# Kernel tuning notes

Measured on AMD Instinct MI355X. Metric: run time of the kernel, lower is better.

Reference implementation:

```python
import jax, jax.numpy as jnp
import numpy as np

SCALE = 0.125  # quantization scale applied inline in the custom matmul
PAD = 4
STRIDE = 1


def setup_inputs() -> dict:
    key = jax.random.key(0)
    k1, k2, k3 = jax.random.split(key, 3)
    x = jax.random.normal(k1, (8, 64, 16384), dtype=jnp.float32)        # (N, C, L)
    weight = jax.random.normal(k2, (64, 64, 9), dtype=jnp.float32) * 0.05  # (O, I, K)
    bias = jax.random.normal(k3, (64,), dtype=jnp.float32)               # (O,)
    return {"x": x, "weight": weight, "bias": bias}


def reference(x, weight, bias):
    # Mathematically identical to: im2col unfold -> (N, out_l, C*K) @ (C*K, O),
    # then out * scale + bias. Expressed as a fused conv to avoid the huge
    # intermediate while computing the same result.
    out = jax.lax.conv_general_dilated(
        x, weight,
        window_strides=(STRIDE,),
        padding=[(PAD, PAD)],
        dimension_numbers=("NCH", "OIH", "NCH"),
    )  # (N, O, out_l)
    return out * SCALE + bias[None, :, None]
```

## Files before the change

kernel.cpp:

```cpp
#include <hip/hip_runtime.h>
#include <hip/hip_bf16.h>

#define C_IN    64
#define L_IN    16384
#define O_OUT   64
#define KTAP    9
#define LTILE   256
#define ROWS    272
#define RSTRIDE 72

typedef short          bf16x8 __attribute__((ext_vector_type(8)));
typedef unsigned short u16x8  __attribute__((ext_vector_type(8)));
typedef unsigned int   u32x4  __attribute__((ext_vector_type(4)));
typedef float          f32x4  __attribute__((ext_vector_type(4)));
typedef float          f32x8v __attribute__((ext_vector_type(8)));

static __device__ __forceinline__ unsigned short f2bf(float f) {
  __hip_bfloat16 h = __float2bfloat16(f);
  return __builtin_bit_cast(unsigned short, h);
}

static __device__ __forceinline__ unsigned int pk2(float lo, float hi) {
  return (unsigned int)f2bf(lo) | ((unsigned int)f2bf(hi) << 16);
}

__global__ void w_rearrange(const float* __restrict__ w,
                            unsigned short* __restrict__ w2) {
    int i = blockIdx.x * 256 + threadIdx.x;
    if (i >= KTAP * O_OUT * C_IN) return;
    int t  = i >> 12;
    int oc = i & 4095;
    w2[i] = f2bf(w[oc * KTAP + t] * 0.125f);
}

__global__ __launch_bounds__(256) void qconv_kernel(
    const float* __restrict__ x,
    const unsigned short* __restrict__ w2,
    const float* __restrict__ bias,
    float* __restrict__ out) {

  __shared__ __align__(16) unsigned short xs[ROWS][RSTRIDE];

  const int tid = threadIdx.x;
  const int n   = blockIdx.x >> 6;
  const int l0  = (blockIdx.x & 63) << 8;
  const float* xn = x + (size_t)n * C_IN * L_IN;

  for (int idx = tid; idx < ROWS; idx += 256) {
    const int cb = idx & 7;
    const int lb = idx >> 3;
    const int c0 = cb << 3;
    const int gl0 = l0 - 8 + (lb << 3);
    if (gl0 >= 0 && gl0 + 8 <= L_IN) {
      f32x8v v[8];
#pragma unroll
      for (int i = 0; i < 8; ++i)
        v[i] = *reinterpret_cast<const f32x8v*>(xn + (size_t)(c0 + i) * L_IN + gl0);
#pragma unroll
      for (int j = 0; j < 8; ++j) {
        u32x4 wv;
#pragma unroll
        for (int p = 0; p < 4; ++p)
          wv[p] = pk2(v[2 * p][j], v[2 * p + 1][j]);
        *reinterpret_cast<u32x4*>(&xs[(lb << 3) + j][c0]) = wv;
      }
    } else {
      unsigned short vb[8][8];
      for (int i = 0; i < 8; ++i)
        for (int j = 0; j < 8; ++j) {
          int gl = gl0 + j;
          vb[i][j] = (gl >= 0 && gl < L_IN)
                         ? f2bf(xn[(size_t)(c0 + i) * L_IN + gl])
                         : (unsigned short)0;
        }
      for (int j = 0; j < 8; ++j) {
        u16x8 wv;
        for (int i = 0; i < 8; ++i) wv[i] = vb[i][j];
        *reinterpret_cast<u16x8*>(&xs[(lb << 3) + j][c0]) = wv;
      }
    }
  }
  __syncthreads();

  const int wave = tid >> 6;
  const int lane = tid & 63;
  const int wr   = wave >> 1;
  const int wc   = wave & 1;
  const int col  = lane & 15;
  const int quad = lane >> 4;

  f32x4 acc[2][8];
#pragma unroll
  for (int m = 0; m < 2; ++m)
#pragma unroll
    for (int lt = 0; lt < 8; ++lt) acc[m][lt] = (f32x4){0.f, 0.f, 0.f, 0.f};

  const int rbase = (wc << 7) + col + 4;

  for (int t = 0; t < KTAP; ++t) {
    bf16x8 a[2][2];
#pragma unroll
    for (int m = 0; m < 2; ++m)
#pragma unroll
      for (int k = 0; k < 2; ++k)
        a[m][k] = *reinterpret_cast<const bf16x8*>(
            w2 + (t << 12) + (((wr << 5) + (m << 4) + col) << 6) + (k << 5) + (quad << 3));

#pragma unroll
    for (int k = 0; k < 2; ++k) {
#pragma unroll
      for (int lt = 0; lt < 8; ++lt) {
        const int r = rbase + t + (lt << 4);
        const bf16x8 b = *reinterpret_cast<const bf16x8*>(&xs[r][(k << 5) + (quad << 3)]);
        acc[0][lt] = __builtin_amdgcn_mfma_f32_16x16x32_bf16(a[0][k], b, acc[0][lt], 0, 0, 0);
        acc[1][lt] = __builtin_amdgcn_mfma_f32_16x16x32_bf16(a[1][k], b, acc[1][lt], 0, 0, 0);
      }
    }
  }

#pragma unroll
  for (int m = 0; m < 2; ++m) {
    const int obase = (wr << 5) + (m << 4) + (quad << 2);
    float bv[4];
#pragma unroll
    for (int reg = 0; reg < 4; ++reg) bv[reg] = bias[obase + reg];
#pragma unroll
    for (int lt = 0; lt < 8; ++lt) {
      const int l = l0 + (wc << 7) + (lt << 4) + col;
#pragma unroll
      for (int reg = 0; reg < 4; ++reg) {
        const int o = obase + reg;
        out[((size_t)(n * O_OUT + o) << 14) + l] = acc[m][lt][reg] + bv[reg];
      }
    }
  }
}

extern "C" void kernel_launch(void* const* d_in, const int* in_sizes, int n_in,
                              void* d_out, int out_size, void* d_ws, size_t ws_size,
                              hipStream_t stream) {
  const float*    x    = (const float*)d_in[0];
  const float*    w    = (const float*)d_in[1];
  const float*    bias = (const float*)d_in[2];
  float*          out  = (float*)d_out;
  unsigned short* w2   = (unsigned short*)d_ws;

  w_rearrange<<<(KTAP * O_OUT * C_IN + 255) / 256, 256, 0, stream>>>(w, w2);

  qconv_kernel<<<8 * (L_IN / LTILE), 256, 0, stream>>>(x, w2, bias, out);
}
```

Before: 98.83 us.

## Split L tile into two halves and overlap second-half staging with first-half MFMAs

```diff
diff --git a/kernel.cpp b/kernel.cpp
--- a/kernel.cpp
+++ b/kernel.cpp
@@ -7,13 +7,12 @@
 #define KTAP    9
 #define LTILE   256
 #define ROWS    272
+#define AROWS   144
 #define RSTRIDE 72
 
 typedef short          bf16x8 __attribute__((ext_vector_type(8)));
-typedef unsigned short u16x8  __attribute__((ext_vector_type(8)));
 typedef unsigned int   u32x4  __attribute__((ext_vector_type(4)));
 typedef float          f32x4  __attribute__((ext_vector_type(4)));
-typedef float          f32x8v __attribute__((ext_vector_type(8)));
 
 static __device__ __forceinline__ unsigned short f2bf(float f) {
   __hip_bfloat16 h = __float2bfloat16(f);
@@ -46,93 +45,165 @@
   const int l0  = (blockIdx.x & 63) << 8;
   const float* xn = x + (size_t)n * C_IN * L_IN;
 
-  for (int idx = tid; idx < ROWS; idx += 256) {
-    const int cb = idx & 7;
-    const int lb = idx >> 3;
-    const int c0 = cb << 3;
-    const int gl0 = l0 - 8 + (lb << 3);
-    if (gl0 >= 0 && gl0 + 8 <= L_IN) {
-      f32x8v v[8];
-#pragma unroll
-      for (int i = 0; i < 8; ++i)
-        v[i] = *reinterpret_cast<const f32x8v*>(xn + (size_t)(c0 + i) * L_IN + gl0);
-#pragma unroll
-      for (int j = 0; j < 8; ++j) {
-        u32x4 wv;
-#pragma unroll
-        for (int p = 0; p < 4; ++p)
-          wv[p] = pk2(v[2 * p][j], v[2 * p + 1][j]);
-        *reinterpret_cast<u32x4*>(&xs[(lb << 3) + j][c0]) = wv;
-      }
-    } else {
-      unsigned short vb[8][8];
-      for (int i = 0; i < 8; ++i)
-        for (int j = 0; j < 8; ++j) {
-          int gl = gl0 + j;
-          vb[i][j] = (gl >= 0 && gl < L_IN)
-                         ? f2bf(xn[(size_t)(c0 + i) * L_IN + gl])
-                         : (unsigned short)0;
+  const int ucb = tid & 7;
+  const int ulb = tid >> 3;
+  const int uc0 = ucb << 3;
+
+  const int a0_gl0 = l0 - 8 + (ulb << 2);
+  const bool a0_ok = (a0_gl0 >= 0) && (a0_gl0 + 4 <= L_IN);
+  f32x4 va0[8];
+  if (a0_ok) {
+#pragma unroll
+    for (int i = 0; i < 8; ++i)
+      va0[i] = *reinterpret_cast<const f32x4*>(xn + (size_t)(uc0 + i) * L_IN + a0_gl0);
+  }
+  const bool have1 = (tid < 32);
+  const int a1_gl0 = l0 - 8 + ((32 + ulb) << 2);
+  f32x4 va1[8];
+  if (have1) {
+#pragma unroll
+    for (int i = 0; i < 8; ++i)
+      va1[i] = *reinterpret_cast<const f32x4*>(xn + (size_t)(uc0 + i) * L_IN + a1_gl0);
+  }
+  const int b_gl0 = l0 + 136 + (ulb << 2);
+  const bool b_ok = (b_gl0 + 4 <= L_IN);
+  f32x4 vb[8];
+  if (b_ok) {
+#pragma unroll
+    for (int i = 0; i < 8; ++i)
+      vb[i] = *reinterpret_cast<const f32x4*>(xn + (size_t)(uc0 + i) * L_IN + b_gl0);
+  }
+
+  if (a0_ok) {
+#pragma unroll
+    for (int j = 0; j < 4; ++j) {
+      u32x4 wv;
+#pragma unroll
+      for (int p = 0; p < 4; ++p)
+        wv[p] = pk2(va0[2 * p][j], va0[2 * p + 1][j]);
+      *reinterpret_cast<u32x4*>(&xs[(ulb << 2) + j][uc0]) = wv;
+    }
+  } else {
+#pragma unroll
+    for (int j = 0; j < 4; ++j) {
+      const int gl = a0_gl0 + j;
+      u32x4 wv;
+#pragma unroll
+      for (int p = 0; p < 4; ++p) {
+        float lo = 0.f, hi = 0.f;
+        if (gl >= 0 && gl < L_IN) {
+          lo = xn[(size_t)(uc0 + 2 * p)     * L_IN + gl];
+          hi = xn[(size_t)(uc0 + 2 * p + 1) * L_IN + gl];
         }
-      for (int j = 0; j < 8; ++j) {
-        u16x8 wv;
-        for (int i = 0; i < 8; ++i) wv[i] = vb[i][j];
-        *reinterpret_cast<u16x8*>(&xs[(lb << 3) + j][c0]) = wv;
-      }
+        wv[p] = pk2(lo, hi);
+      }
+      *reinterpret_cast<u32x4*>(&xs[(ulb << 2) + j][uc0]) = wv;
+    }
+  }
+  if (have1) {
+#pragma unroll
+    for (int j = 0; j < 4; ++j) {
+      u32x4 wv;
+#pragma unroll
+      for (int p = 0; p < 4; ++p)
+        wv[p] = pk2(va1[2 * p][j], va1[2 * p + 1][j]);
+      *reinterpret_cast<u32x4*>(&xs[128 + (ulb << 2) + j][uc0]) = wv;
     }
   }
   __syncthreads();
 
   const int wave = tid >> 6;
   const int lane = tid & 63;
-  const int wr   = wave >> 1;
-  const int wc   = wave & 1;
   const int col  = lane & 15;
   const int quad = lane >> 4;
 
-  f32x4 acc[2][8];
-#pragma unroll
-  for (int m = 0; m < 2; ++m)
-#pragma unroll
-    for (int lt = 0; lt < 8; ++lt) acc[m][lt] = (f32x4){0.f, 0.f, 0.f, 0.f};
-
-  const int rbase = (wc << 7) + col + 4;
+  const unsigned short* wbase = w2 + (((wave << 4) + col) << 6) + (quad << 3);
+  const int obase = (wave << 4) + (quad << 2);
+  float bv[4];
+#pragma unroll
+  for (int reg = 0; reg < 4; ++reg) bv[reg] = bias[obase + reg];
+
+  f32x4 acc[8];
+#pragma unroll
+  for (int lt = 0; lt < 8; ++lt) acc[lt] = (f32x4){0.f, 0.f, 0.f, 0.f};
 
   for (int t = 0; t < KTAP; ++t) {
-    bf16x8 a[2][2];
-#pragma unroll
-    for (int m = 0; m < 2; ++m)
-#pragma unroll
-      for (int k = 0; k < 2; ++k)
-        a[m][k] = *reinterpret_cast<const bf16x8*>(
-            w2 + (t << 12) + (((wr << 5) + (m << 4) + col) << 6) + (k << 5) + (quad << 3));
-
+    bf16x8 a[2];
+#pragma unroll
+    for (int k = 0; k < 2; ++k)
+      a[k] = *reinterpret_cast<const bf16x8*>(wbase + (t << 12) + (k << 5));
 #pragma unroll
     for (int k = 0; k < 2; ++k) {
 #pragma unroll
       for (int lt = 0; lt < 8; ++lt) {
-        const int r = rbase + t + (lt << 4);
+        const int r = col + t + 4 + (lt << 4);
         const bf16x8 b = *reinterpret_cast<const bf16x8*>(&xs[r][(k << 5) + (quad << 3)]);
-        acc[0][lt] = __builtin_amdgcn_mfma_f32_16x16x32_bf16(a[0][k], b, acc[0][lt], 0, 0, 0);
-        acc[1][lt] = __builtin_amdgcn_mfma_f32_16x16x32_bf16(a[1][k], b, acc[1][lt], 0, 0, 0);
-      }
-    }
-  }
-
-#pragma unroll
-  for (int m = 0; m < 2; ++m) {
-    const int obase = (wr << 5) + (m << 4) + (quad << 2);
-    float bv[4];
-#pragma unroll
-    for (int reg = 0; reg < 4; ++reg) bv[reg] = bias[obase + reg];
-#pragma unroll
-    for (int lt = 0; lt < 8; ++lt) {
-      const int l = l0 + (wc << 7) + (lt << 4) + col;
-#pragma unroll
-      for (int reg = 0; reg < 4; ++reg) {
-        const int o = obase + reg;
-        out[((size_t)(n * O_OUT + o) << 14) + l] = acc[m][lt][reg] + bv[reg];
-      }
-    }
+        acc[lt] = __builtin_amdgcn_mfma_f32_16x16x32_bf16(a[k], b, acc[lt], 0, 0, 0);
+      }
+    }
+  }
+
+  if (b_ok) {
+#pragma unroll
+    for (int j = 0; j < 4; ++j) {
+      u32x4 wv;
+#pragma unroll
+      for (int p = 0; p < 4; ++p)
+        wv[p] = pk2(vb[2 * p][j], vb[2 * p + 1][j]);
+      *reinterpret_cast<u32x4*>(&xs[144 + (ulb << 2) + j][uc0]) = wv;
+    }
+  } else {
+#pragma unroll
+    for (int j = 0; j < 4; ++j) {
+      const int gl = b_gl0 + j;
+      u32x4 wv;
+#pragma unroll
+      for (int p = 0; p < 4; ++p) {
+        float lo = 0.f, hi = 0.f;
+        if (gl < L_IN) {
+          lo = xn[(size_t)(uc0 + 2 * p)     * L_IN + gl];
+          hi = xn[(size_t)(uc0 + 2 * p + 1) * L_IN + gl];
+        }
+        wv[p] = pk2(lo, hi);
+      }
+      *reinterpret_cast<u32x4*>(&xs[144 + (ulb << 2) + j][uc0]) = wv;
+    }
+  }
+  __syncthreads();
+
+#pragma unroll
+  for (int lt = 0; lt < 8; ++lt) {
+    const int l = l0 + (lt << 4) + col;
+#pragma unroll
+    for (int reg = 0; reg < 4; ++reg)
+      out[((size_t)(n * O_OUT + obase + reg) << 14) + l] = acc[lt][reg] + bv[reg];
+  }
+
+#pragma unroll
+  for (int lt = 0; lt < 8; ++lt) acc[lt] = (f32x4){0.f, 0.f, 0.f, 0.f};
+
+  for (int t = 0; t < KTAP; ++t) {
+    bf16x8 a[2];
+#pragma unroll
+    for (int k = 0; k < 2; ++k)
+      a[k] = *reinterpret_cast<const bf16x8*>(wbase + (t << 12) + (k << 5));
+#pragma unroll
+    for (int k = 0; k < 2; ++k) {
+#pragma unroll
+      for (int lt = 0; lt < 8; ++lt) {
+        const int r = 128 + col + t + 4 + (lt << 4);
+        const bf16x8 b = *reinterpret_cast<const bf16x8*>(&xs[r][(k << 5) + (quad << 3)]);
+        acc[lt] = __builtin_amdgcn_mfma_f32_16x16x32_bf16(a[k], b, acc[lt], 0, 0, 0);
+      }
+    }
+  }
+
+#pragma unroll
+  for (int lt = 0; lt < 8; ++lt) {
+    const int l = l0 + 128 + (lt << 4) + col;
+#pragma unroll
+    for (int reg = 0; reg < 4; ++reg)
+      out[((size_t)(n * O_OUT + obase + reg) << 14) + l] = acc[lt][reg] + bv[reg];
   }
 }
 
```

New measurement: 98.00 us. About the same (-0.8%).

## Fuse weight conversion into conv kernel and keep weight fragments in registers

Applied to the files above, without the earlier changes.

```diff
diff --git a/kernel.cpp b/kernel.cpp
--- a/kernel.cpp
+++ b/kernel.cpp
@@ -24,18 +24,9 @@
   return (unsigned int)f2bf(lo) | ((unsigned int)f2bf(hi) << 16);
 }
 
-__global__ void w_rearrange(const float* __restrict__ w,
-                            unsigned short* __restrict__ w2) {
-    int i = blockIdx.x * 256 + threadIdx.x;
-    if (i >= KTAP * O_OUT * C_IN) return;
-    int t  = i >> 12;
-    int oc = i & 4095;
-    w2[i] = f2bf(w[oc * KTAP + t] * 0.125f);
-}
-
 __global__ __launch_bounds__(256) void qconv_kernel(
     const float* __restrict__ x,
-    const unsigned short* __restrict__ w2,
+    const float* __restrict__ w,
     const float* __restrict__ bias,
     float* __restrict__ out) {
 
@@ -81,71 +72,105 @@
     }
   }
   __syncthreads();
+  __builtin_amdgcn_sched_barrier(0);
 
   const int wave = tid >> 6;
   const int lane = tid & 63;
-  const int wr   = wave >> 1;
-  const int wc   = wave & 1;
   const int col  = lane & 15;
   const int quad = lane >> 4;
+  const int o16  = (wave << 4) + col;
 
-  f32x4 acc[2][8];
+  u32x4 afr[2 * KTAP];
+  {
+    const float* wrow = w + (size_t)o16 * (C_IN * KTAP);
 #pragma unroll
-  for (int m = 0; m < 2; ++m)
+    for (int k = 0; k < 2; ++k) {
+      const float* wp = wrow + ((k << 5) + (quad << 3)) * KTAP;
+      f32x4 wt[18];
 #pragma unroll
-    for (int lt = 0; lt < 8; ++lt) acc[m][lt] = (f32x4){0.f, 0.f, 0.f, 0.f};
+      for (int j = 0; j < 18; ++j)
+        wt[j] = *reinterpret_cast<const f32x4*>(wp + 4 * j);
+#pragma unroll
+      for (int t = 0; t < KTAP; ++t) {
+        u32x4 fr;
+#pragma unroll
+        for (int p = 0; p < 4; ++p) {
+          const int e0 = (2 * p) * KTAP + t;
+          const int e1 = (2 * p + 1) * KTAP + t;
+          fr[p] = pk2(wt[e0 >> 2][e0 & 3] * 0.125f,
+                      wt[e1 >> 2][e1 & 3] * 0.125f);
+        }
+        afr[(t << 1) + k] = fr;
+      }
+    }
+  }
+  __builtin_amdgcn_sched_barrier(0);
 
-  const int rbase = (wc << 7) + col + 4;
+  const int obase = (wave << 4) + (quad << 2);
+  float bv[4];
+#pragma unroll
+  for (int reg = 0; reg < 4; ++reg) bv[reg] = bias[obase + reg];
 
-  for (int t = 0; t < KTAP; ++t) {
-    bf16x8 a[2][2];
+  f32x4 acc[8];
 #pragma unroll
-    for (int m = 0; m < 2; ++m)
-#pragma unroll
-      for (int k = 0; k < 2; ++k)
-        a[m][k] = *reinterpret_cast<const bf16x8*>(
-            w2 + (t << 12) + (((wr << 5) + (m << 4) + col) << 6) + (k << 5) + (quad << 3));
+  for (int lt = 0; lt < 8; ++lt) acc[lt] = (f32x4){0.f, 0.f, 0.f, 0.f};
 
 #pragma unroll
+  for (int t = 0; t < KTAP; ++t) {
+#pragma unroll
     for (int k = 0; k < 2; ++k) {
+      const bf16x8 a = __builtin_bit_cast(bf16x8, afr[(t << 1) + k]);
 #pragma unroll
       for (int lt = 0; lt < 8; ++lt) {
-        const int r = rbase + t + (lt << 4);
+        const int r = col + t + 4 + (lt << 4);
         const bf16x8 b = *reinterpret_cast<const bf16x8*>(&xs[r][(k << 5) + (quad << 3)]);
-        acc[0][lt] = __builtin_amdgcn_mfma_f32_16x16x32_bf16(a[0][k], b, acc[0][lt], 0, 0, 0);
-        acc[1][lt] = __builtin_amdgcn_mfma_f32_16x16x32_bf16(a[1][k], b, acc[1][lt], 0, 0, 0);
+        acc[lt] = __builtin_amdgcn_mfma_f32_16x16x32_bf16(a, b, acc[lt], 0, 0, 0);
       }
     }
   }
 
 #pragma unroll
-  for (int m = 0; m < 2; ++m) {
-    const int obase = (wr << 5) + (m << 4) + (quad << 2);
-    float bv[4];
+  for (int lt = 0; lt < 8; ++lt) {
+    const int l = l0 + (lt << 4) + col;
 #pragma unroll
-    for (int reg = 0; reg < 4; ++reg) bv[reg] = bias[obase + reg];
+    for (int reg = 0; reg < 4; ++reg)
+      out[((size_t)(n * O_OUT + obase + reg) << 14) + l] = acc[lt][reg] + bv[reg];
+  }
+
 #pragma unroll
-    for (int lt = 0; lt < 8; ++lt) {
-      const int l = l0 + (wc << 7) + (lt << 4) + col;
+  for (int lt = 0; lt < 8; ++lt) acc[lt] = (f32x4){0.f, 0.f, 0.f, 0.f};
+
 #pragma unroll
-      for (int reg = 0; reg < 4; ++reg) {
-        const int o = obase + reg;
-        out[((size_t)(n * O_OUT + o) << 14) + l] = acc[m][lt][reg] + bv[reg];
+  for (int t = 0; t < KTAP; ++t) {
+#pragma unroll
+    for (int k = 0; k < 2; ++k) {
+      const bf16x8 a = __builtin_bit_cast(bf16x8, afr[(t << 1) + k]);
+#pragma unroll
+      for (int lt = 0; lt < 8; ++lt) {
+        const int r = 128 + col + t + 4 + (lt << 4);
+        const bf16x8 b = *reinterpret_cast<const bf16x8*>(&xs[r][(k << 5) + (quad << 3)]);
+        acc[lt] = __builtin_amdgcn_mfma_f32_16x16x32_bf16(a, b, acc[lt], 0, 0, 0);
       }
     }
+  }
+
+#pragma unroll
+  for (int lt = 0; lt < 8; ++lt) {
+    const int l = l0 + 128 + (lt << 4) + col;
+#pragma unroll
+    for (int reg = 0; reg < 4; ++reg)
+      out[((size_t)(n * O_OUT + obase + reg) << 14) + l] = acc[lt][reg] + bv[reg];
   }
 }
 
 extern "C" void kernel_launch(void* const* d_in, const int* in_sizes, int n_in,
                               void* d_out, int out_size, void* d_ws, size_t ws_size,
                               hipStream_t stream) {
-  const float*    x    = (const float*)d_in[0];
-  const float*    w    = (const float*)d_in[1];
-  const float*    bias = (const float*)d_in[2];
-  float*          out  = (float*)d_out;
-  unsigned short* w2   = (unsigned short*)d_ws;
+  const float* x    = (const float*)d_in[0];
+  const float* w    = (const float*)d_in[1];
+  const float* bias = (const float*)d_in[2];
+  float*       out  = (float*)d_out;
+  (void)d_ws; (void)ws_size;
 
-  w_rearrange<<<(KTAP * O_OUT * C_IN + 255) / 256, 256, 0, stream>>>(w, w2);
-
-  qconv_kernel<<<8 * (L_IN / LTILE), 256, 0, stream>>>(x, w2, bias, out);
+  qconv_kernel<<<8 * (L_IN / LTILE), 256, 0, stream>>>(x, w, bias, out);
 }
```

New measurement: 102.8 us. 1.04x slower.
